# Performance work log

Measured on AMD Instinct MI355X. Metric: run time of the kernel, lower is better.

## Reference

```python
import jax, jax.numpy as jnp
import numpy as np

GD, D, S, L = 14, 128, 16, 2  # gaussian_dim, hidden_dim, d_state, num_layers


def _layernorm(x, g, b):
    m = x.mean(-1, keepdims=True)
    v = ((x - m) ** 2).mean(-1, keepdims=True)
    return (x - m) / jnp.sqrt(v + 1e-5) * g + b


def _scan_dir(x, dtW, dtb, BW, CW, Alog, Dskip):
    # x: [M, N, D]. Diagonal selective SSM, one direction.
    dt = jax.nn.softplus(x @ dtW + dtb)          # [M, N, D]
    Bm = x @ BW                                   # [M, N, S]
    Cm = x @ CW                                   # [M, N, S]
    A = -jnp.exp(Alog)                            # [D, S]

    def step(s, inp):
        x_t, dt_t, B_t, C_t = inp                 # [M,D],[M,D],[M,S],[M,S]
        s = jnp.exp(A * dt_t[:, :, None]) * s + (dt_t * x_t)[:, :, None] * B_t[:, None, :]
        y = jnp.einsum('mds,ms->md', s, C_t) + Dskip * x_t
        return s, y

    s0 = jnp.zeros((x.shape[0], D, S), x.dtype)
    _, ys = jax.lax.scan(step, s0, (x.transpose(1, 0, 2), dt.transpose(1, 0, 2),
                                    Bm.transpose(1, 0, 2), Cm.transpose(1, 0, 2)))
    return ys.transpose(1, 0, 2)                  # [M, N, D]


def setup_inputs() -> dict:
    key = jax.random.key(0)
    ks = jax.random.split(key, 20)
    N, B, P = 8, 1, 20000
    inp = {}
    inp['xyz'] = jax.random.normal(ks[0], (N, B, P, 3), jnp.float32)
    inp['scale'] = jax.random.normal(ks[1], (N, B, P, 3), jnp.float32)
    inp['rotation'] = jax.random.normal(ks[2], (N, B, P, 4), jnp.float32)
    inp['opacity'] = jax.random.normal(ks[3], (N, B, P, 1), jnp.float32)
    inp['color'] = jax.random.normal(ks[4], (N, B, P, 3), jnp.float32)
    inp['t'] = jnp.array([0.37], jnp.float32)
    inp['timestamps'] = jnp.linspace(0.0, 1.0, N, dtype=jnp.float32)

    def lin(k, i, o):
        return (jax.random.normal(k, (i, o), jnp.float32) / np.sqrt(i)).astype(jnp.float32)

    inp['in_W'] = lin(ks[5], GD, D); inp['in_b'] = jnp.zeros((D,), jnp.float32)
    inp['ln_g'] = jnp.ones((L, D), jnp.float32); inp['ln_b'] = jnp.zeros((L, D), jnp.float32)
    inp['dt_W'] = jax.random.normal(ks[6], (L, 2, D, D), jnp.float32) / np.sqrt(D)
    inp['dt_b'] = jnp.zeros((L, 2, D), jnp.float32)
    inp['B_W'] = jax.random.normal(ks[7], (L, 2, D, S), jnp.float32) / np.sqrt(D)
    inp['C_W'] = jax.random.normal(ks[8], (L, 2, D, S), jnp.float32) / np.sqrt(D)
    inp['A_log'] = jnp.log(jax.random.uniform(ks[9], (L, 2, D, S), jnp.float32, 0.5, 2.0))
    inp['D_skip'] = jnp.ones((L, 2, D), jnp.float32)
    inp['out_W'] = jax.random.normal(ks[10], (L, 2 * D, D), jnp.float32) / np.sqrt(2 * D)
    inp['out_b'] = jnp.zeros((L, D), jnp.float32)
    inp['te_W1'] = jax.random.normal(ks[11], (1, D), jnp.float32)
    inp['te_b1'] = jnp.zeros((D,), jnp.float32)
    inp['te_W2'] = jax.random.normal(ks[12], (D, D), jnp.float32) / np.sqrt(D)
    inp['te_b2'] = jnp.zeros((D,), jnp.float32)
    inp['op_W'] = jax.random.normal(ks[13], (D, GD), jnp.float32) / np.sqrt(D)
    inp['op_b'] = jnp.zeros((GD,), jnp.float32)
    return inp


def reference(xyz, scale, rotation, opacity, color, t, timestamps,
              in_W, in_b, ln_g, ln_b, dt_W, dt_b, B_W, C_W, A_log, D_skip,
              out_W, out_b, te_W1, te_b1, te_W2, te_b2, op_W, op_b):
    N, B, P = xyz.shape[0], xyz.shape[1], xyz.shape[2]
    M = B * P
    # stack frames: [N,B,P,14] -> [B*P, N, 14]
    params = jnp.concatenate([xyz, scale, rotation, opacity, color], -1)
    params = params.transpose(1, 2, 0, 3).reshape(M, N, GD)
    h = params @ in_W + in_b                      # [M, N, D]
    # sinusoidal temporal position encoding from continuous timestamps
    ts = jnp.broadcast_to(timestamps[None, :], (M, N))
    half = D // 2
    freqs = jnp.exp(-jnp.log(10000.0) * jnp.arange(half, dtype=h.dtype) / half)
    ang = ts[..., None] * freqs                   # [M, N, D/2]
    h = h + jnp.concatenate([jnp.sin(ang), jnp.cos(ang)], -1)
    # bidirectional SSM layers (pre-LN, residual)
    for l in range(L):
        xn = _layernorm(h, ln_g[l], ln_b[l])
        yf = _scan_dir(xn, dt_W[l, 0], dt_b[l, 0], B_W[l, 0], C_W[l, 0], A_log[l, 0], D_skip[l, 0])
        yb = jnp.flip(_scan_dir(jnp.flip(xn, 1), dt_W[l, 1], dt_b[l, 1], B_W[l, 1], C_W[l, 1],
                                A_log[l, 1], D_skip[l, 1]), 1)
        h = h + jnp.concatenate([yf, yb], -1) @ out_W[l] + out_b[l]
    # temporal query: linear interpolation between neighboring hidden states
    t_full = jnp.broadcast_to(t.reshape(B, 1), (B, P)).reshape(M)
    tn = t_full * (N - 1)
    idx_low = jnp.clip(jnp.floor(tn).astype(jnp.int32), 0, N - 2)
    idx_high = jnp.minimum(idx_low + 1, N - 1)
    alpha = (tn - idx_low.astype(h.dtype))[:, None]
    rows = jnp.arange(M)
    h_low = h[rows, idx_low]                      # [M, D]
    h_high = h[rows, idx_high]
    h_i = (1.0 - alpha) * h_low + alpha * h_high
    te = jax.nn.silu(t_full[:, None] @ te_W1 + te_b1) @ te_W2 + te_b2
    h_i = h_i + te
    out = (h_i @ op_W + op_b).reshape(B, P, GD)
    xyz_o = out[..., :3]
    scale_o = jax.nn.softplus(out[..., 3:6])
    rot = out[..., 6:10]
    rot_o = rot / jnp.clip(jnp.linalg.norm(rot, axis=-1, keepdims=True), 1e-12)
    opac_o = jax.nn.sigmoid(out[..., 10:11])
    col_o = jax.nn.sigmoid(out[..., 11:14])
    # dict fields concatenated in canonical order -> [B, P, 14]
    return jnp.concatenate([xyz_o, scale_o, rot_o, opac_o, col_o], -1)
```

## Files before the change

### kernel.cpp

```cpp
#include <hip/hip_runtime.h>
#include <math.h>

#define DD   128
#define SS   16
#define NL   2
#define GDIM 14
#define NN   8

typedef short  s16x8 __attribute__((ext_vector_type(8)));
typedef float  f32x4 __attribute__((ext_vector_type(4)));
typedef unsigned short ushort_t;

#define WS_INW   0
#define WS_DTW   4096
#define WS_BCW   69632
#define WS_OUTW  86016
#define WS_USH   151552
#define WS_AFLT  8192
#define WS_PEB   8192
#define WS_TE    9216

#if __has_builtin(__builtin_amdgcn_exp2f)
#define EXP2(x) __builtin_amdgcn_exp2f(x)
#else
#define EXP2(x) exp2f(x)
#endif

__device__ __forceinline__ unsigned short f2bf(float f) {
    unsigned u = __float_as_uint(f);
    u += 0x7fffu + ((u >> 16) & 1u);
    return (unsigned short)(u >> 16);
}

__device__ __forceinline__ float softplus_fast(float x) {
    return fmaxf(x, 0.f) + __logf(1.f + __expf(-fabsf(x)));
}
__device__ __forceinline__ float softplus_precise(float x) {
    return fmaxf(x, 0.f) + log1pf(expf(-fabsf(x)));
}

extern "C" __global__ void __launch_bounds__(256)
prep_weights(const float* __restrict__ inW, const float* __restrict__ dtW,
             const float* __restrict__ BW,  const float* __restrict__ CW,
             const float* __restrict__ outW, const float* __restrict__ Alog,
             const float* __restrict__ tstamp, const float* __restrict__ inB,
             const float* __restrict__ t_arr,
             const float* __restrict__ teW1, const float* __restrict__ teB1,
             const float* __restrict__ teW2, const float* __restrict__ teB2,
             int Bcnt, ushort_t* __restrict__ ws)
{
    float* wsf = (float*)(ws + WS_USH);
    int i = blockIdx.x * 256 + threadIdx.x;
    if (i < 4096) {
        int d = i >> 5, k = i & 31;
        ws[WS_INW + i] = (k < GDIM) ? f2bf(inW[k * DD + d]) : (ushort_t)0;
        return;
    }
    i -= 4096;
    if (i < 65536) {
        int l = i >> 15, r = i & 32767;
        int col = r >> 7, k = r & 127;
        int dir = col >> 7, d = col & 127;
        ws[WS_DTW + i] = f2bf(dtW[((size_t)(l * 2 + dir) * DD + k) * DD + d]);
        return;
    }
    i -= 65536;
    if (i < 16384) {
        int l = i >> 13, r = i & 8191;
        int col = r >> 7, k = r & 127;
        int dir = col >> 5, which = (col >> 4) & 1, s = col & 15;
        const float* Wsrc = which ? CW : BW;
        ws[WS_BCW + i] = f2bf(Wsrc[((size_t)(l * 2 + dir) * DD + k) * SS + s]);
        return;
    }
    i -= 16384;
    if (i < 65536) {
        int l = i >> 15, r = i & 32767;
        int col = r >> 8, k = r & 255;
        ws[WS_OUTW + i] = f2bf(outW[((size_t)l * 2 * DD + k) * DD + col]);
        return;
    }
    i -= 65536;
    if (i < WS_AFLT) {
        int ld = i >> 11, r = i & 2047;
        int s = r >> 7, d = r & 127;
        wsf[i] = -expf(Alog[((size_t)ld * DD + d) * SS + s]) * 1.44269504088896f;
        return;
    }
    i -= WS_AFLT;
    if (i < 1024) {
        int n = i >> 7, d = i & 127;
        int j = d & 63;
        float freq = expf(-logf(10000.f) * (float)j * (1.f / 64.f));
        float ang = tstamp[n] * freq;
        wsf[WS_PEB + i] = inB[d] + ((d < 64) ? sinf(ang) : cosf(ang));
        return;
    }
    i -= 1024;
    if (i < Bcnt * 128) {
        int b = i >> 7, d = i & 127;
        float tv = t_arr[b];
        float acc = teB2[d];
        for (int k = 0; k < DD; ++k) {
            float u = fmaf(tv, teW1[k], teB1[k]);
            float s = u / (1.f + expf(-u));
            acc = fmaf(s, teW2[k * DD + d], acc);
        }
        wsf[WS_TE + i] = acc;
    }
}

extern "C" __global__ void __launch_bounds__(256, 5)
ssm_mfma(const float* __restrict__ xyz, const float* __restrict__ scl,
         const float* __restrict__ rotp, const float* __restrict__ opa,
         const float* __restrict__ colp,
         const float* __restrict__ t_arr,
         const float* __restrict__ lnG, const float* __restrict__ lnB,
         const float* __restrict__ dtB,
         const float* __restrict__ Dskp,
         const float* __restrict__ outB,
         const float* __restrict__ opW, const float* __restrict__ opB,
         const ushort_t* __restrict__ wsu,
         float* __restrict__ out, int M, int Pb)
{
    const int t    = threadIdx.x;
    const int lane = t & 63;
    const int wv   = t >> 6;
    const int d    = t & 127;
    const int p    = t >> 7;
    const int m0   = blockIdx.x * 2;
    const int m    = m0 + p;
    const int r16  = lane & 15;
    const int kg   = lane >> 4;

    __shared__ float arenaA[16][132];
    __shared__ float arenaB[16][260];
    __shared__ float red  [4][2][NN];

    float (*pres)[132] = arenaA;
    ushort_t* XsU = (ushort_t*)&arenaA[0][0];
    float (*bcres)[68] = (float(*)[68])&arenaA[0][0];
    float (*dtres)[260] = arenaB;
    ushort_t* YsU = (ushort_t*)&arenaB[0][0];

    const ushort_t* inWt  = wsu + WS_INW;
    const ushort_t* dtWt  = wsu + WS_DTW;
    const ushort_t* bcWt  = wsu + WS_BCW;
    const ushort_t* outWt = wsu + WS_OUTW;
    const float*    wsf   = (const float*)(wsu + WS_USH);
    const float*    Apre  = wsf;
    const float*    peb   = wsf + WS_PEB;
    const float*    te    = wsf + WS_TE;

    for (int idx = t; idx < 16 * 32; idx += 256) {
        const int row = idx >> 5, k = idx & 31;
        const int pp = row >> 3, n = row & 7;
        const int mm = m0 + pp;
        float v = 0.f;
        if (k < GDIM && mm < M) {
            if (k < 3)       v = xyz [((size_t)n * M + mm) * 3 + k];
            else if (k < 6)  v = scl [((size_t)n * M + mm) * 3 + (k - 3)];
            else if (k < 10) v = rotp[((size_t)n * M + mm) * 4 + (k - 6)];
            else if (k < 11) v = opa [ (size_t)n * M + mm];
            else             v = colp[((size_t)n * M + mm) * 3 + (k - 11)];
        }
        XsU[row * 264 + k] = f2bf(v);
    }
    __syncthreads();

    {
        const s16x8 a = *(const s16x8*)&XsU[r16 * 264 + kg * 8];
        __syncthreads();
        #pragma unroll
        for (int ti = 0; ti < 2; ++ti) {
            const int col = (wv * 2 + ti) * 16 + r16;
            const s16x8 b = *(const s16x8*)&inWt[col * 32 + kg * 8];
            f32x4 acc = {0.f, 0.f, 0.f, 0.f};
            acc = __builtin_amdgcn_mfma_f32_16x16x32_bf16(a, b, acc, 0, 0, 0);
            #pragma unroll
            for (int j = 0; j < 4; ++j) pres[kg * 4 + j][col] = acc[j];
        }
    }
    __syncthreads();

    float h[NN];
    #pragma unroll
    for (int n = 0; n < NN; ++n)
        h[n] = pres[p * 8 + n][d] + peb[n * DD + d];

    for (int l = 0; l < NL; ++l) {
        float sum[NN], sq[NN];
        #pragma unroll
        for (int n = 0; n < NN; ++n) { sum[n] = h[n]; sq[n] = h[n] * h[n]; }
        #pragma unroll
        for (int off = 32; off > 0; off >>= 1) {
            #pragma unroll
            for (int n = 0; n < NN; ++n) {
                sum[n] += __shfl_xor(sum[n], off);
                sq[n]  += __shfl_xor(sq[n],  off);
            }
        }
        if (lane == 0) {
            #pragma unroll
            for (int n = 0; n < NN; ++n) { red[wv][0][n] = sum[n]; red[wv][1][n] = sq[n]; }
        }
        __syncthreads();

        float xn[NN];
        {
            const float gg = lnG[l * DD + d], bb = lnB[l * DD + d];
            #pragma unroll
            for (int n = 0; n < NN; ++n) {
                const float s0 = red[2 * p][0][n] + red[2 * p + 1][0][n];
                const float s1 = red[2 * p][1][n] + red[2 * p + 1][1][n];
                const float mean = s0 * (1.f / 128.f);
                float var = s1 * (1.f / 128.f) - mean * mean;
                const float inv = rsqrtf(fmaxf(var, 0.f) + 1e-5f);
                xn[n] = fmaf((h[n] - mean) * inv, gg, bb);
                XsU[(p * 8 + n) * 264 + d] = f2bf(xn[n]);
            }
        }
        __syncthreads();

        {
            s16x8 a[4];
            #pragma unroll
            for (int kc = 0; kc < 4; ++kc)
                a[kc] = *(const s16x8*)&XsU[r16 * 264 + kc * 32 + kg * 8];
            __syncthreads();

            const ushort_t* dtl = dtWt + l * 32768;
            #pragma unroll
            for (int ti = 0; ti < 4; ++ti) {
                const int col = (wv * 4 + ti) * 16 + r16;
                f32x4 acc = {0.f, 0.f, 0.f, 0.f};
                #pragma unroll
                for (int kc = 0; kc < 4; ++kc) {
                    const s16x8 b = *(const s16x8*)&dtl[col * 128 + kc * 32 + kg * 8];
                    acc = __builtin_amdgcn_mfma_f32_16x16x32_bf16(a[kc], b, acc, 0, 0, 0);
                }
                #pragma unroll
                for (int j = 0; j < 4; ++j) dtres[kg * 4 + j][col] = acc[j];
            }
            const ushort_t* bcl = bcWt + l * 8192;
            {
                const int col = wv * 16 + r16;
                f32x4 acc = {0.f, 0.f, 0.f, 0.f};
                #pragma unroll
                for (int kc = 0; kc < 4; ++kc) {
                    const s16x8 b = *(const s16x8*)&bcl[col * 128 + kc * 32 + kg * 8];
                    acc = __builtin_amdgcn_mfma_f32_16x16x32_bf16(a[kc], b, acc, 0, 0, 0);
                }
                #pragma unroll
                for (int j = 0; j < 4; ++j) bcres[kg * 4 + j][col] = acc[j];
            }
        }
        __syncthreads();

        float dtv[2][NN];
        #pragma unroll
        for (int dir = 0; dir < 2; ++dir) {
            const float db = dtB[(l * 2 + dir) * DD + d];
            #pragma unroll
            for (int n = 0; n < NN; ++n)
                dtv[dir][n] = softplus_fast(dtres[p * 8 + n][dir * 128 + d] + db);
        }
        __syncthreads();

        #pragma unroll
        for (int dir = 0; dir < 2; ++dir) {
            const float* Ap = Apre + (size_t)(l * 2 + dir) * SS * DD + d;
            float Ar[SS];
            #pragma unroll
            for (int s = 0; s < SS; ++s) Ar[s] = Ap[s * DD];
            const float dsk = Dskp[(l * 2 + dir) * DD + d];
            float st[SS];
            #pragma unroll
            for (int s = 0; s < SS; ++s) st[s] = 0.f;
            #pragma unroll
            for (int t8 = 0; t8 < NN; ++t8) {
                const int n = dir ? (NN - 1 - t8) : t8;
                const float dtc = dtv[dir][n];
                const float xv  = xn[n];
                const float dx  = dtc * xv;
                float y = dsk * xv;
                const float* base = &bcres[p * 8 + n][dir * 32];
                #pragma unroll
                for (int s4 = 0; s4 < SS; s4 += 4) {
                    const float4 Bv = *(const float4*)&base[s4];
                    const float4 Cv = *(const float4*)&base[16 + s4];
                    st[s4+0] = fmaf(EXP2(Ar[s4+0] * dtc), st[s4+0], dx * Bv.x);
                    y = fmaf(st[s4+0], Cv.x, y);
                    st[s4+1] = fmaf(EXP2(Ar[s4+1] * dtc), st[s4+1], dx * Bv.y);
                    y = fmaf(st[s4+1], Cv.y, y);
                    st[s4+2] = fmaf(EXP2(Ar[s4+2] * dtc), st[s4+2], dx * Bv.z);
                    y = fmaf(st[s4+2], Cv.z, y);
                    st[s4+3] = fmaf(EXP2(Ar[s4+3] * dtc), st[s4+3], dx * Bv.w);
                    y = fmaf(st[s4+3], Cv.w, y);
                }
                YsU[(p * 8 + n) * 520 + dir * 128 + d] = f2bf(y);
            }
        }
        __syncthreads();

        {
            s16x8 a[8];
            #pragma unroll
            for (int kc = 0; kc < 8; ++kc)
                a[kc] = *(const s16x8*)&YsU[r16 * 520 + kc * 32 + kg * 8];
            const ushort_t* ol = outWt + l * 32768;
            #pragma unroll
            for (int ti = 0; ti < 2; ++ti) {
                const int col = (wv * 2 + ti) * 16 + r16;
                f32x4 acc = {0.f, 0.f, 0.f, 0.f};
                #pragma unroll
                for (int kc = 0; kc < 8; ++kc) {
                    const s16x8 b = *(const s16x8*)&ol[col * 256 + kc * 32 + kg * 8];
                    acc = __builtin_amdgcn_mfma_f32_16x16x32_bf16(a[kc], b, acc, 0, 0, 0);
                }
                #pragma unroll
                for (int j = 0; j < 4; ++j) pres[kg * 4 + j][col] = acc[j];
            }
        }
        __syncthreads();

        {
            const float ob = outB[l * DD + d];
            #pragma unroll
            for (int n = 0; n < NN; ++n) h[n] += pres[p * 8 + n][d] + ob;
        }
    }

    const int mc = (m < M) ? m : (M - 1);
    const int bidx = mc / Pb;
    const float tv = t_arr[bidx];
    const float tn = tv * (float)(NN - 1);
    int il = (int)floorf(tn);
    il = il < 0 ? 0 : (il > NN - 2 ? NN - 2 : il);
    const float alpha = tn - (float)il;
    float hlow = 0.f, hhigh = 0.f;
    #pragma unroll
    for (int n = 0; n < NN; ++n) {
        if (n == il)     hlow  = h[n];
        if (n == il + 1) hhigh = h[n];
    }
    float hi = (1.f - alpha) * hlow + alpha * hhigh + te[bidx * DD + d];

    float* epi = &arenaB[0][0];
    epi[p * 132 + d] = hi;
    __syncthreads();

    if (d < GDIM * 8) {
        const int g = d >> 3, j = d & 7;
        float part = 0.f;
        #pragma unroll
        for (int q = 0; q < 16; ++q)
            part = fmaf(epi[p * 132 + j + 8 * q], opW[(j + 8 * q) * GDIM + g], part);
        part += __shfl_xor(part, 4);
        part += __shfl_xor(part, 2);
        part += __shfl_xor(part, 1);
        if (j == 0) epi[264 + p * 16 + g] = part + opB[g];
    }
    __syncthreads();

    if (d < GDIM && m < M) {
        const int g = d;
        const float v = epi[264 + p * 16 + g];
        float r;
        if (g < 3)        r = v;
        else if (g < 6)   r = softplus_precise(v);
        else if (g < 10) {
            const float q0 = epi[264 + p * 16 + 6], q1 = epi[264 + p * 16 + 7];
            const float q2 = epi[264 + p * 16 + 8], q3 = epi[264 + p * 16 + 9];
            const float nrm = sqrtf(fmaf(q0,q0, fmaf(q1,q1, fmaf(q2,q2, q3*q3))));
            r = v / fmaxf(nrm, 1e-12f);
        } else {
            r = 1.f / (1.f + expf(-v));
        }
        out[(size_t)m * GDIM + g] = r;
    }
}

extern "C" void kernel_launch(void* const* d_in, const int* in_sizes, int n_in,
                              void* d_out, int out_size, void* d_ws, size_t ws_size,
                              hipStream_t stream) {
    const float* xyz   = (const float*)d_in[0];
    const float* scl   = (const float*)d_in[1];
    const float* rotp  = (const float*)d_in[2];
    const float* opa   = (const float*)d_in[3];
    const float* colp  = (const float*)d_in[4];
    const float* t_arr = (const float*)d_in[5];
    const float* tstmp = (const float*)d_in[6];
    const float* inW   = (const float*)d_in[7];
    const float* inB   = (const float*)d_in[8];
    const float* lnG   = (const float*)d_in[9];
    const float* lnB   = (const float*)d_in[10];
    const float* dtW   = (const float*)d_in[11];
    const float* dtB   = (const float*)d_in[12];
    const float* BW    = (const float*)d_in[13];
    const float* CW    = (const float*)d_in[14];
    const float* Alog  = (const float*)d_in[15];
    const float* Dskp  = (const float*)d_in[16];
    const float* outW  = (const float*)d_in[17];
    const float* outB  = (const float*)d_in[18];
    const float* teW1  = (const float*)d_in[19];
    const float* teB1  = (const float*)d_in[20];
    const float* teW2  = (const float*)d_in[21];
    const float* teB2  = (const float*)d_in[22];
    const float* opW   = (const float*)d_in[23];
    const float* opB   = (const float*)d_in[24];

    const int N  = in_sizes[6];
    const int M  = in_sizes[3] / N;
    const int B  = in_sizes[5];
    const int Pb = M / B;
    (void)N; (void)out_size; (void)n_in;

    ushort_t* wsu = (ushort_t*)d_ws;
    const int prep_elems = WS_USH + WS_AFLT + 1024 + B * 128;
    hipLaunchKernelGGL(prep_weights, dim3((prep_elems + 255) / 256), dim3(256), 0, stream,
                       inW, dtW, BW, CW, outW, Alog, tstmp, inB, t_arr,
                       teW1, teB1, teW2, teB2, B, wsu);
    hipLaunchKernelGGL(ssm_mfma, dim3((M + 1) / 2), dim3(256), 0, stream,
                       xyz, scl, rotp, opa, colp, t_arr,
                       lnG, lnB, dtB, Dskp, outB, opW, opB,
                       wsu, (float*)d_out, M, Pb);
}
```

Baseline: 591.0 us.

## Split fused SSM kernel into staged front, scan, mid, and tail kernels

Replaces the single fused per-point kernel with a pipeline of five launches (front projection and layernorm, per-layer scan, mid out-projection and layernorm, tail interpolation and head). Intermediates such as hidden state, normalized input, dt, B/C and scan outputs go through global scratch in the workspace, processed in chunks that fit the available space. The aim is to let each stage run at its own occupancy and register budget instead of one heavy kernel. The cost is extra global memory traffic and more kernel launches. The original fused kernel is kept as a fallback when the workspace is too small.

New measurement: 801.2 us. +35.6%, slower.

```diff
diff --git a/kernel.cpp b/kernel.cpp
--- a/kernel.cpp
+++ b/kernel.cpp
@@ -31,7 +31,9 @@
     u += 0x7fffu + ((u >> 16) & 1u);
     return (unsigned short)(u >> 16);
 }
-
+__device__ __forceinline__ float bf2f(ushort_t u) {
+    return __uint_as_float(((unsigned)u) << 16);
+}
 __device__ __forceinline__ float softplus_fast(float x) {
     return fmaxf(x, 0.f) + __logf(1.f + __expf(-fabsf(x)));
 }
@@ -110,18 +112,481 @@
     }
 }
 
-extern "C" __global__ void __launch_bounds__(256, 5)
-ssm_mfma(const float* __restrict__ xyz, const float* __restrict__ scl,
+
+extern "C" __global__ void __launch_bounds__(256, 4)
+k1_front(const float* __restrict__ xyz, const float* __restrict__ scl,
          const float* __restrict__ rotp, const float* __restrict__ opa,
          const float* __restrict__ colp,
-         const float* __restrict__ t_arr,
          const float* __restrict__ lnG, const float* __restrict__ lnB,
-         const float* __restrict__ dtB,
-         const float* __restrict__ Dskp,
-         const float* __restrict__ outB,
-         const float* __restrict__ opW, const float* __restrict__ opB,
          const ushort_t* __restrict__ wsu,
-         float* __restrict__ out, int M, int Pb)
+         float* __restrict__ Hb, ushort_t* __restrict__ XNb,
+         float* __restrict__ DTb, float* __restrict__ BCb,
+         int M, int Mc, int m_off)
+{
+    const int t    = threadIdx.x;
+    const int lane = t & 63;
+    const int wv   = t >> 6;
+    const int d    = t & 127;
+    const int p    = t >> 7;
+    const int lm0  = blockIdx.x * 2;
+    const int lm   = lm0 + p;
+    const int m0   = m_off + lm0;
+    const int r16  = lane & 15;
+    const int kg   = lane >> 4;
+
+    __shared__ float arenaA[16][132];
+    __shared__ float red[4][2][NN];
+    float (*pres)[132] = arenaA;
+    ushort_t* XsU = (ushort_t*)&arenaA[0][0];
+
+    const ushort_t* inWt = wsu + WS_INW;
+    const ushort_t* dtWt = wsu + WS_DTW;
+    const ushort_t* bcWt = wsu + WS_BCW;
+    const float*    wsf  = (const float*)(wsu + WS_USH);
+    const float*    peb  = wsf + WS_PEB;
+
+    for (int idx = t; idx < 16 * 32; idx += 256) {
+        const int row = idx >> 5, k = idx & 31;
+        const int pp = row >> 3, n = row & 7;
+        const int mm = m0 + pp;
+        float v = 0.f;
+        if (k < GDIM && mm < M) {
+            if (k < 3)       v = xyz [((size_t)n * M + mm) * 3 + k];
+            else if (k < 6)  v = scl [((size_t)n * M + mm) * 3 + (k - 3)];
+            else if (k < 10) v = rotp[((size_t)n * M + mm) * 4 + (k - 6)];
+            else if (k < 11) v = opa [ (size_t)n * M + mm];
+            else             v = colp[((size_t)n * M + mm) * 3 + (k - 11)];
+        }
+        XsU[row * 264 + k] = f2bf(v);
+    }
+    __syncthreads();
+
+    {
+        const s16x8 a = *(const s16x8*)&XsU[r16 * 264 + kg * 8];
+        __syncthreads();
+        #pragma unroll
+        for (int ti = 0; ti < 2; ++ti) {
+            const int col = (wv * 2 + ti) * 16 + r16;
+            const s16x8 b = *(const s16x8*)&inWt[col * 32 + kg * 8];
+            f32x4 acc = {0.f, 0.f, 0.f, 0.f};
+            acc = __builtin_amdgcn_mfma_f32_16x16x32_bf16(a, b, acc, 0, 0, 0);
+            #pragma unroll
+            for (int j = 0; j < 4; ++j) pres[kg * 4 + j][col] = acc[j];
+        }
+    }
+    __syncthreads();
+
+    float h[NN];
+    #pragma unroll
+    for (int n = 0; n < NN; ++n) {
+        h[n] = pres[p * 8 + n][d] + peb[n * DD + d];
+        Hb[((size_t)n * Mc + lm) * DD + d] = h[n];
+    }
+
+    float sum[NN], sq[NN];
+    #pragma unroll
+    for (int n = 0; n < NN; ++n) { sum[n] = h[n]; sq[n] = h[n] * h[n]; }
+    #pragma unroll
+    for (int off = 32; off > 0; off >>= 1) {
+        #pragma unroll
+        for (int n = 0; n < NN; ++n) {
+            sum[n] += __shfl_xor(sum[n], off);
+            sq[n]  += __shfl_xor(sq[n],  off);
+        }
+    }
+    if (lane == 0) {
+        #pragma unroll
+        for (int n = 0; n < NN; ++n) { red[wv][0][n] = sum[n]; red[wv][1][n] = sq[n]; }
+    }
+    __syncthreads();
+
+    {
+        const float gg = lnG[d], bb = lnB[d];
+        #pragma unroll
+        for (int n = 0; n < NN; ++n) {
+            const float s0 = red[2 * p][0][n] + red[2 * p + 1][0][n];
+            const float s1 = red[2 * p][1][n] + red[2 * p + 1][1][n];
+            const float mean = s0 * (1.f / 128.f);
+            float var = s1 * (1.f / 128.f) - mean * mean;
+            const float inv = rsqrtf(fmaxf(var, 0.f) + 1e-5f);
+            const float xnv = fmaf((h[n] - mean) * inv, gg, bb);
+            const ushort_t xb = f2bf(xnv);
+            XsU[(p * 8 + n) * 264 + d] = xb;
+            XNb[((size_t)n * Mc + lm) * DD + d] = xb;
+        }
+    }
+    __syncthreads();
+
+    {
+        s16x8 a[4];
+        #pragma unroll
+        for (int kc = 0; kc < 4; ++kc)
+            a[kc] = *(const s16x8*)&XsU[r16 * 264 + kc * 32 + kg * 8];
+
+        const ushort_t* dtl = dtWt;
+        #pragma unroll
+        for (int ti = 0; ti < 4; ++ti) {
+            const int col = (wv * 4 + ti) * 16 + r16;
+            f32x4 acc = {0.f, 0.f, 0.f, 0.f};
+            #pragma unroll
+            for (int kc = 0; kc < 4; ++kc) {
+                const s16x8 b = *(const s16x8*)&dtl[col * 128 + kc * 32 + kg * 8];
+                acc = __builtin_amdgcn_mfma_f32_16x16x32_bf16(a[kc], b, acc, 0, 0, 0);
+            }
+            #pragma unroll
+            for (int j = 0; j < 4; ++j) {
+                const int row = kg * 4 + j;
+                const int lmr = lm0 + (row >> 3), nr = row & 7;
+                DTb[((size_t)nr * Mc + lmr) * 256 + col] = acc[j];
+            }
+        }
+        const ushort_t* bcl = bcWt;
+        {
+            const int col = wv * 16 + r16;
+            f32x4 acc = {0.f, 0.f, 0.f, 0.f};
+            #pragma unroll
+            for (int kc = 0; kc < 4; ++kc) {
+                const s16x8 b = *(const s16x8*)&bcl[col * 128 + kc * 32 + kg * 8];
+                acc = __builtin_amdgcn_mfma_f32_16x16x32_bf16(a[kc], b, acc, 0, 0, 0);
+            }
+            #pragma unroll
+            for (int j = 0; j < 4; ++j) {
+                const int row = kg * 4 + j;
+                const int lmr = lm0 + (row >> 3), nr = row & 7;
+                BCb[((size_t)lmr * 8 + nr) * 64 + col] = acc[j];
+            }
+        }
+    }
+}
+
+extern "C" __global__ void __launch_bounds__(256, 5)
+k2_scan(const ushort_t* __restrict__ wsu,
+        const ushort_t* __restrict__ XNb, const float* __restrict__ DTb,
+        const float* __restrict__ BCb, ushort_t* __restrict__ YB,
+        const float* __restrict__ dtB, const float* __restrict__ Dskp,
+        int Mc, int l)
+{
+    const int t  = threadIdx.x;
+    const int d  = t & 127;
+    const int p  = t >> 7;
+    const int lm = blockIdx.x * 2 + p;
+
+    __shared__ float bcs[1024];
+    {
+        float4* dst = (float4*)bcs;
+        const float4* src = (const float4*)(BCb + (size_t)blockIdx.x * 1024);
+        dst[t] = src[t];
+    }
+    __syncthreads();
+
+    const float* wsf  = (const float*)(wsu + WS_USH);
+    const float* Apre = wsf;
+
+    float dtv[2][NN];
+    #pragma unroll
+    for (int dir = 0; dir < 2; ++dir) {
+        const float db = dtB[(l * 2 + dir) * DD + d];
+        #pragma unroll
+        for (int n = 0; n < NN; ++n)
+            dtv[dir][n] = softplus_fast(DTb[((size_t)n * Mc + lm) * 256 + dir * 128 + d] + db);
+    }
+    float xn[NN];
+    #pragma unroll
+    for (int n = 0; n < NN; ++n)
+        xn[n] = bf2f(XNb[((size_t)n * Mc + lm) * DD + d]);
+
+    #pragma unroll
+    for (int dir = 0; dir < 2; ++dir) {
+        const float* Ap = Apre + (size_t)(l * 2 + dir) * SS * DD + d;
+        float Ar[SS];
+        #pragma unroll
+        for (int s = 0; s < SS; ++s) Ar[s] = Ap[s * DD];
+        const float dsk = Dskp[(l * 2 + dir) * DD + d];
+        float st[SS];
+        #pragma unroll
+        for (int s = 0; s < SS; ++s) st[s] = 0.f;
+        #pragma unroll
+        for (int t8 = 0; t8 < NN; ++t8) {
+            const int n = dir ? (NN - 1 - t8) : t8;
+            const float dtc = dtv[dir][n];
+            const float xv  = xn[n];
+            const float dx  = dtc * xv;
+            float y = dsk * xv;
+            const float* base = &bcs[p * 512 + n * 64 + dir * 32];
+            #pragma unroll
+            for (int s4 = 0; s4 < SS; s4 += 4) {
+                const float4 Bv = *(const float4*)&base[s4];
+                const float4 Cv = *(const float4*)&base[16 + s4];
+                st[s4+0] = fmaf(EXP2(Ar[s4+0] * dtc), st[s4+0], dx * Bv.x);
+                y = fmaf(st[s4+0], Cv.x, y);
+                st[s4+1] = fmaf(EXP2(Ar[s4+1] * dtc), st[s4+1], dx * Bv.y);
+                y = fmaf(st[s4+1], Cv.y, y);
+                st[s4+2] = fmaf(EXP2(Ar[s4+2] * dtc), st[s4+2], dx * Bv.z);
+                y = fmaf(st[s4+2], Cv.z, y);
+                st[s4+3] = fmaf(EXP2(Ar[s4+3] * dtc), st[s4+3], dx * Bv.w);
+                y = fmaf(st[s4+3], Cv.w, y);
+            }
+            YB[((size_t)n * Mc + lm) * 256 + dir * 128 + d] = f2bf(y);
+        }
+    }
+}
+
+extern "C" __global__ void __launch_bounds__(256, 4)
+k3_mid(const ushort_t* __restrict__ wsu,
+       float* __restrict__ Hb, ushort_t* __restrict__ XNb,
+       float* __restrict__ DTb, float* __restrict__ BCb,
+       const ushort_t* __restrict__ YB,
+       const float* __restrict__ outB,
+       const float* __restrict__ lnG, const float* __restrict__ lnB,
+       int Mc, int lout, int lin)
+{
+    const int t    = threadIdx.x;
+    const int lane = t & 63;
+    const int wv   = t >> 6;
+    const int d    = t & 127;
+    const int p    = t >> 7;
+    const int lm0  = blockIdx.x * 2;
+    const int lm   = lm0 + p;
+    const int r16  = lane & 15;
+    const int kg   = lane >> 4;
+
+    __shared__ float arenaA[16][132];
+    __shared__ float red[4][2][NN];
+    float (*pres)[132] = arenaA;
+    ushort_t* XsU = (ushort_t*)&arenaA[0][0];
+
+    const ushort_t* dtWt  = wsu + WS_DTW;
+    const ushort_t* bcWt  = wsu + WS_BCW;
+    const ushort_t* outWt = wsu + WS_OUTW;
+
+    {
+        const int prow = r16 >> 3, nrow = r16 & 7;
+        const size_t grow = (size_t)nrow * Mc + (lm0 + prow);
+        s16x8 a[8];
+        #pragma unroll
+        for (int kc = 0; kc < 8; ++kc)
+            a[kc] = *(const s16x8*)&YB[grow * 256 + kc * 32 + kg * 8];
+        const ushort_t* ol = outWt + lout * 32768;
+        #pragma unroll
+        for (int ti = 0; ti < 2; ++ti) {
+            const int col = (wv * 2 + ti) * 16 + r16;
+            f32x4 acc = {0.f, 0.f, 0.f, 0.f};
+            #pragma unroll
+            for (int kc = 0; kc < 8; ++kc) {
+                const s16x8 b = *(const s16x8*)&ol[col * 256 + kc * 32 + kg * 8];
+                acc = __builtin_amdgcn_mfma_f32_16x16x32_bf16(a[kc], b, acc, 0, 0, 0);
+            }
+            #pragma unroll
+            for (int j = 0; j < 4; ++j) pres[kg * 4 + j][col] = acc[j];
+        }
+    }
+    __syncthreads();
+
+    float h[NN];
+    {
+        const float ob = outB[lout * DD + d];
+        #pragma unroll
+        for (int n = 0; n < NN; ++n) {
+            h[n] = Hb[((size_t)n * Mc + lm) * DD + d] + pres[p * 8 + n][d] + ob;
+            Hb[((size_t)n * Mc + lm) * DD + d] = h[n];
+        }
+    }
+
+    float sum[NN], sq[NN];
+    #pragma unroll
+    for (int n = 0; n < NN; ++n) { sum[n] = h[n]; sq[n] = h[n] * h[n]; }
+    #pragma unroll
+    for (int off = 32; off > 0; off >>= 1) {
+        #pragma unroll
+        for (int n = 0; n < NN; ++n) {
+            sum[n] += __shfl_xor(sum[n], off);
+            sq[n]  += __shfl_xor(sq[n],  off);
+        }
+    }
+    if (lane == 0) {
+        #pragma unroll
+        for (int n = 0; n < NN; ++n) { red[wv][0][n] = sum[n]; red[wv][1][n] = sq[n]; }
+    }
+    __syncthreads();
+
+    {
+        const float gg = lnG[lin * DD + d], bb = lnB[lin * DD + d];
+        #pragma unroll
+        for (int n = 0; n < NN; ++n) {
+            const float s0 = red[2 * p][0][n] + red[2 * p + 1][0][n];
+            const float s1 = red[2 * p][1][n] + red[2 * p + 1][1][n];
+            const float mean = s0 * (1.f / 128.f);
+            float var = s1 * (1.f / 128.f) - mean * mean;
+            const float inv = rsqrtf(fmaxf(var, 0.f) + 1e-5f);
+            const float xnv = fmaf((h[n] - mean) * inv, gg, bb);
+            const ushort_t xb = f2bf(xnv);
+            XsU[(p * 8 + n) * 264 + d] = xb;
+            XNb[((size_t)n * Mc + lm) * DD + d] = xb;
+        }
+    }
+    __syncthreads();
+
+    {
+        s16x8 a[4];
+        #pragma unroll
+        for (int kc = 0; kc < 4; ++kc)
+            a[kc] = *(const s16x8*)&XsU[r16 * 264 + kc * 32 + kg * 8];
+
+        const ushort_t* dtl = dtWt + lin * 32768;
+        #pragma unroll
+        for (int ti = 0; ti < 4; ++ti) {
+            const int col = (wv * 4 + ti) * 16 + r16;
+            f32x4 acc = {0.f, 0.f, 0.f, 0.f};
+            #pragma unroll
+            for (int kc = 0; kc < 4; ++kc) {
+                const s16x8 b = *(const s16x8*)&dtl[col * 128 + kc * 32 + kg * 8];
+                acc = __builtin_amdgcn_mfma_f32_16x16x32_bf16(a[kc], b, acc, 0, 0, 0);
+            }
+            #pragma unroll
+            for (int j = 0; j < 4; ++j) {
+                const int row = kg * 4 + j;
+                const int lmr = lm0 + (row >> 3), nr = row & 7;
+                DTb[((size_t)nr * Mc + lmr) * 256 + col] = acc[j];
+            }
+        }
+        const ushort_t* bcl = bcWt + lin * 8192;
+        {
+            const int col = wv * 16 + r16;
+            f32x4 acc = {0.f, 0.f, 0.f, 0.f};
+            #pragma unroll
+            for (int kc = 0; kc < 4; ++kc) {
+                const s16x8 b = *(const s16x8*)&bcl[col * 128 + kc * 32 + kg * 8];
+                acc = __builtin_amdgcn_mfma_f32_16x16x32_bf16(a[kc], b, acc, 0, 0, 0);
+            }
+            #pragma unroll
+            for (int j = 0; j < 4; ++j) {
+                const int row = kg * 4 + j;
+                const int lmr = lm0 + (row >> 3), nr = row & 7;
+                BCb[((size_t)lmr * 8 + nr) * 64 + col] = acc[j];
+            }
+        }
+    }
+}
+
+extern "C" __global__ void __launch_bounds__(256, 4)
+k5_tail(const ushort_t* __restrict__ wsu,
+        const float* __restrict__ Hb, const ushort_t* __restrict__ YB,
+        const float* __restrict__ outB, const float* __restrict__ t_arr,
+        const float* __restrict__ opW, const float* __restrict__ opB,
+        float* __restrict__ out, int M, int Mc, int m_off, int Pb, int lout)
+{
+    const int t    = threadIdx.x;
+    const int lane = t & 63;
+    const int wv   = t >> 6;
+    const int d    = t & 127;
+    const int p    = t >> 7;
+    const int lm0  = blockIdx.x * 2;
+    const int lm   = lm0 + p;
+    const int m    = m_off + lm;
+    const int r16  = lane & 15;
+    const int kg   = lane >> 4;
+
+    __shared__ float arenaA[16][132];
+    float (*pres)[132] = arenaA;
+    float* epi = &arenaA[0][0];
+
+    const ushort_t* outWt = wsu + WS_OUTW;
+    const float*    wsf   = (const float*)(wsu + WS_USH);
+    const float*    te    = wsf + WS_TE;
+
+    {
+        const int prow = r16 >> 3, nrow = r16 & 7;
+        const size_t grow = (size_t)nrow * Mc + (lm0 + prow);
+        s16x8 a[8];
+        #pragma unroll
+        for (int kc = 0; kc < 8; ++kc)
+            a[kc] = *(const s16x8*)&YB[grow * 256 + kc * 32 + kg * 8];
+        const ushort_t* ol = outWt + lout * 32768;
+        #pragma unroll
+        for (int ti = 0; ti < 2; ++ti) {
+            const int col = (wv * 2 + ti) * 16 + r16;
+            f32x4 acc = {0.f, 0.f, 0.f, 0.f};
+            #pragma unroll
+            for (int kc = 0; kc < 8; ++kc) {
+                const s16x8 b = *(const s16x8*)&ol[col * 256 + kc * 32 + kg * 8];
+                acc = __builtin_amdgcn_mfma_f32_16x16x32_bf16(a[kc], b, acc, 0, 0, 0);
+            }
+            #pragma unroll
+            for (int j = 0; j < 4; ++j) pres[kg * 4 + j][col] = acc[j];
+        }
+    }
+    __syncthreads();
+
+    float h[NN];
+    {
+        const float ob = outB[lout * DD + d];
+        #pragma unroll
+        for (int n = 0; n < NN; ++n)
+            h[n] = Hb[((size_t)n * Mc + lm) * DD + d] + pres[p * 8 + n][d] + ob;
+    }
+
+    const int mc_   = (m < M) ? m : (M - 1);
+    const int bidx  = mc_ / Pb;
+    const float tv  = t_arr[bidx];
+    const float tn  = tv * (float)(NN - 1);
+    int il = (int)floorf(tn);
+    il = il < 0 ? 0 : (il > NN - 2 ? NN - 2 : il);
+    const float alpha = tn - (float)il;
+    float hlow = 0.f, hhigh = 0.f;
+    #pragma unroll
+    for (int n = 0; n < NN; ++n) {
+        if (n == il)     hlow  = h[n];
+        if (n == il + 1) hhigh = h[n];
+    }
+    float hi = (1.f - alpha) * hlow + alpha * hhigh + te[bidx * DD + d];
+
+    __syncthreads();
+    epi[p * 132 + d] = hi;
+    __syncthreads();
+
+    if (d < GDIM * 8) {
+        const int g = d >> 3, j = d & 7;
+        float part = 0.f;
+        #pragma unroll
+        for (int q = 0; q < 16; ++q)
+            part = fmaf(epi[p * 132 + j + 8 * q], opW[(j + 8 * q) * GDIM + g], part);
+        part += __shfl_xor(part, 4);
+        part += __shfl_xor(part, 2);
+        part += __shfl_xor(part, 1);
+        if (j == 0) epi[264 + p * 16 + g] = part + opB[g];
+    }
+    __syncthreads();
+
+    if (d < GDIM && m < M) {
+        const int g = d;
+        const float v = epi[264 + p * 16 + g];
+        float r;
+        if (g < 3)        r = v;
+        else if (g < 6)   r = softplus_precise(v);
+        else if (g < 10) {
+            const float q0 = epi[264 + p * 16 + 6], q1 = epi[264 + p * 16 + 7];
+            const float q2 = epi[264 + p * 16 + 8], q3 = epi[264 + p * 16 + 9];
+            const float nrm = sqrtf(fmaf(q0,q0, fmaf(q1,q1, fmaf(q2,q2, q3*q3))));
+            r = v / fmaxf(nrm, 1e-12f);
+        } else {
+            r = 1.f / (1.f + expf(-v));
+        }
+        out[(size_t)m * GDIM + g] = r;
+    }
+}
+
+extern "C" __global__ void __launch_bounds__(256, 4)
+ssm_fused_fb(const float* __restrict__ xyz, const float* __restrict__ scl,
+             const float* __restrict__ rotp, const float* __restrict__ opa,
+             const float* __restrict__ colp,
+             const float* __restrict__ t_arr,
+             const float* __restrict__ lnG, const float* __restrict__ lnB,
+             const float* __restrict__ dtB,
+             const float* __restrict__ Dskp,
+             const float* __restrict__ outB,
+             const float* __restrict__ opW, const float* __restrict__ opB,
+             const ushort_t* __restrict__ wsu,
+             float* __restrict__ out, int M, int Pb)
 {
     const int t    = threadIdx.x;
     const int lane = t & 63;
@@ -417,12 +882,50 @@
     (void)N; (void)out_size; (void)n_in;
 
     ushort_t* wsu = (ushort_t*)d_ws;
+
     const int prep_elems = WS_USH + WS_AFLT + 1024 + B * 128;
     hipLaunchKernelGGL(prep_weights, dim3((prep_elems + 255) / 256), dim3(256), 0, stream,
                        inW, dtW, BW, CW, outW, Alog, tstmp, inB, t_arr,
                        teW1, teB1, teW2, teB2, B, wsu);
-    hipLaunchKernelGGL(ssm_mfma, dim3((M + 1) / 2), dim3(256), 0, stream,
-                       xyz, scl, rotp, opa, colp, t_arr,
-                       lnG, lnB, dtB, Dskp, outB, opW, opB,
-                       wsu, (float*)d_out, M, Pb);
-}
+
+    const size_t fixed_bytes  = 303104 + (size_t)(WS_AFLT + 1024 + (size_t)B * 128) * 4;
+    const size_t scratch_off  = (fixed_bytes + 4095) & ~(size_t)4095;
+    const size_t per_pt       = 4096 + 2048 + 8192 + 2048 + 4096;
+    const size_t avail        = ws_size > scratch_off ? ws_size - scratch_off : 0;
+    const int    M_even       = (M + 1) & ~1;
+    size_t mc_cap = avail / per_pt;
+    if (mc_cap > (size_t)M_even) mc_cap = (size_t)M_even;
+    int Mc = (int)(mc_cap & ~(size_t)1);
+
+    if (Mc >= 2048 || Mc >= M_even) {
+        char* s = (char*)d_ws + scratch_off;
+        float*    Hb  = (float*)s;
+        ushort_t* XNb = (ushort_t*)(s + (size_t)Mc * 4096);
+        float*    DTb = (float*)(s + (size_t)Mc * 6144);
+        float*    BCb = (float*)(s + (size_t)Mc * 14336);
+        ushort_t* YB  = (ushort_t*)(s + (size_t)Mc * 16384);
+
+        for (int off = 0; off < M; off += Mc) {
+            const int Mcur = (M - off < Mc) ? (M - off) : Mc;
+            const int Me   = (Mcur + 1) & ~1;
+            const int nb   = Me / 2;
+            hipLaunchKernelGGL(k1_front, dim3(nb), dim3(256), 0, stream,
+                               xyz, scl, rotp, opa, colp, lnG, lnB, wsu,
+                               Hb, XNb, DTb, BCb, M, Mc, off);
+            hipLaunchKernelGGL(k2_scan, dim3(nb), dim3(256), 0, stream,
+                               wsu, XNb, DTb, BCb, YB, dtB, Dskp, Mc, 0);
+            hipLaunchKernelGGL(k3_mid, dim3(nb), dim3(256), 0, stream,
+                               wsu, Hb, XNb, DTb, BCb, YB, outB, lnG, lnB, Mc, 0, 1);
+            hipLaunchKernelGGL(k2_scan, dim3(nb), dim3(256), 0, stream,
+                               wsu, XNb, DTb, BCb, YB, dtB, Dskp, Mc, 1);
+            hipLaunchKernelGGL(k5_tail, dim3(nb), dim3(256), 0, stream,
+                               wsu, Hb, YB, outB, t_arr, opW, opB,
+                               (float*)d_out, M, Mc, off, Pb, 1);
+        }
+    } else {
+        hipLaunchKernelGGL(ssm_fused_fb, dim3((M + 1) / 2), dim3(256), 0, stream,
+                           xyz, scl, rotp, opa, colp, t_arr,
+                           lnG, lnB, dtB, Dskp, outB, opW, opB,
+                           wsu, (float*)d_out, M, Pb);
+    }
+}
```

## Process one particle per 128-thread block instead of two per 256-thread block

Applied to the files above, without the earlier changes.

Each block now handles a single particle sequence, launching M blocks of 128 threads with halved shared-memory arenas. The MFMA A operand duplicates the 8 valid rows into the 16-row tile, and only half the result rows are stored. The aim is smaller blocks and lower shared-memory use, for more resident blocks and finer scheduling. The cost is that half of every matrix-core tile is wasted, and weight loads per particle double.

After: 737.5 us. 24.8% more time.

```diff
diff --git a/kernel.cpp b/kernel.cpp
--- a/kernel.cpp
+++ b/kernel.cpp
@@ -110,7 +110,7 @@
     }
 }
 
-extern "C" __global__ void __launch_bounds__(256, 5)
+extern "C" __global__ void __launch_bounds__(128, 4)
 ssm_mfma(const float* __restrict__ xyz, const float* __restrict__ scl,
          const float* __restrict__ rotp, const float* __restrict__ opa,
          const float* __restrict__ colp,
@@ -126,16 +126,15 @@
     const int t    = threadIdx.x;
     const int lane = t & 63;
     const int wv   = t >> 6;
-    const int d    = t & 127;
-    const int p    = t >> 7;
-    const int m0   = blockIdx.x * 2;
-    const int m    = m0 + p;
+    const int d    = t;
+    const int m    = blockIdx.x;
     const int r16  = lane & 15;
+    const int r8   = lane & 7;
     const int kg   = lane >> 4;
 
-    __shared__ float arenaA[16][132];
-    __shared__ float arenaB[16][260];
-    __shared__ float red  [4][2][NN];
+    __shared__ float arenaA[8][132];
+    __shared__ float arenaB[8][260];
+    __shared__ float red  [2][2][NN];
 
     float (*pres)[132] = arenaA;
     ushort_t* XsU = (ushort_t*)&arenaA[0][0];
@@ -152,33 +151,33 @@
     const float*    peb   = wsf + WS_PEB;
     const float*    te    = wsf + WS_TE;
 
-    for (int idx = t; idx < 16 * 32; idx += 256) {
-        const int row = idx >> 5, k = idx & 31;
-        const int pp = row >> 3, n = row & 7;
-        const int mm = m0 + pp;
+    for (int idx = t; idx < 8 * 32; idx += 128) {
+        const int n = idx >> 5, k = idx & 31;
         float v = 0.f;
-        if (k < GDIM && mm < M) {
-            if (k < 3)       v = xyz [((size_t)n * M + mm) * 3 + k];
-            else if (k < 6)  v = scl [((size_t)n * M + mm) * 3 + (k - 3)];
-            else if (k < 10) v = rotp[((size_t)n * M + mm) * 4 + (k - 6)];
-            else if (k < 11) v = opa [ (size_t)n * M + mm];
-            else             v = colp[((size_t)n * M + mm) * 3 + (k - 11)];
-        }
-        XsU[row * 264 + k] = f2bf(v);
+        if (k < GDIM && m < M) {
+            if (k < 3)       v = xyz [((size_t)n * M + m) * 3 + k];
+            else if (k < 6)  v = scl [((size_t)n * M + m) * 3 + (k - 3)];
+            else if (k < 10) v = rotp[((size_t)n * M + m) * 4 + (k - 6)];
+            else if (k < 11) v = opa [ (size_t)n * M + m];
+            else             v = colp[((size_t)n * M + m) * 3 + (k - 11)];
+        }
+        XsU[n * 264 + k] = f2bf(v);
     }
     __syncthreads();
 
     {
-        const s16x8 a = *(const s16x8*)&XsU[r16 * 264 + kg * 8];
-        __syncthreads();
-        #pragma unroll
-        for (int ti = 0; ti < 2; ++ti) {
-            const int col = (wv * 2 + ti) * 16 + r16;
+        const s16x8 a = *(const s16x8*)&XsU[r8 * 264 + kg * 8];
+        __syncthreads();
+        #pragma unroll
+        for (int ti = 0; ti < 4; ++ti) {
+            const int col = (wv * 4 + ti) * 16 + r16;
             const s16x8 b = *(const s16x8*)&inWt[col * 32 + kg * 8];
             f32x4 acc = {0.f, 0.f, 0.f, 0.f};
             acc = __builtin_amdgcn_mfma_f32_16x16x32_bf16(a, b, acc, 0, 0, 0);
-            #pragma unroll
-            for (int j = 0; j < 4; ++j) pres[kg * 4 + j][col] = acc[j];
+            if (kg < 2) {
+                #pragma unroll
+                for (int j = 0; j < 4; ++j) pres[kg * 4 + j][col] = acc[j];
+            }
         }
     }
     __syncthreads();
@@ -186,7 +185,7 @@
     float h[NN];
     #pragma unroll
     for (int n = 0; n < NN; ++n)
-        h[n] = pres[p * 8 + n][d] + peb[n * DD + d];
+        h[n] = pres[n][d] + peb[n * DD + d];
 
     for (int l = 0; l < NL; ++l) {
         float sum[NN], sq[NN];
@@ -211,13 +210,13 @@
             const float gg = lnG[l * DD + d], bb = lnB[l * DD + d];
             #pragma unroll
             for (int n = 0; n < NN; ++n) {
-                const float s0 = red[2 * p][0][n] + red[2 * p + 1][0][n];
-                const float s1 = red[2 * p][1][n] + red[2 * p + 1][1][n];
+                const float s0 = red[0][0][n] + red[1][0][n];
+                const float s1 = red[0][1][n] + red[1][1][n];
                 const float mean = s0 * (1.f / 128.f);
                 float var = s1 * (1.f / 128.f) - mean * mean;
                 const float inv = rsqrtf(fmaxf(var, 0.f) + 1e-5f);
                 xn[n] = fmaf((h[n] - mean) * inv, gg, bb);
-                XsU[(p * 8 + n) * 264 + d] = f2bf(xn[n]);
+                XsU[n * 264 + d] = f2bf(xn[n]);
             }
         }
         __syncthreads();
@@ -226,33 +225,38 @@
             s16x8 a[4];
             #pragma unroll
             for (int kc = 0; kc < 4; ++kc)
-                a[kc] = *(const s16x8*)&XsU[r16 * 264 + kc * 32 + kg * 8];
+                a[kc] = *(const s16x8*)&XsU[r8 * 264 + kc * 32 + kg * 8];
             __syncthreads();
 
             const ushort_t* dtl = dtWt + l * 32768;
             #pragma unroll
-            for (int ti = 0; ti < 4; ++ti) {
-                const int col = (wv * 4 + ti) * 16 + r16;
+            for (int ti = 0; ti < 8; ++ti) {
+                const int col = (wv * 8 + ti) * 16 + r16;
                 f32x4 acc = {0.f, 0.f, 0.f, 0.f};
                 #pragma unroll
                 for (int kc = 0; kc < 4; ++kc) {
                     const s16x8 b = *(const s16x8*)&dtl[col * 128 + kc * 32 + kg * 8];
                     acc = __builtin_amdgcn_mfma_f32_16x16x32_bf16(a[kc], b, acc, 0, 0, 0);
                 }
-                #pragma unroll
-                for (int j = 0; j < 4; ++j) dtres[kg * 4 + j][col] = acc[j];
+                if (kg < 2) {
+                    #pragma unroll
+                    for (int j = 0; j < 4; ++j) dtres[kg * 4 + j][col] = acc[j];
+                }
             }
             const ushort_t* bcl = bcWt + l * 8192;
-            {
-                const int col = wv * 16 + r16;
+            #pragma unroll
+            for (int ti = 0; ti < 2; ++ti) {
+                const int col = (wv * 2 + ti) * 16 + r16;
                 f32x4 acc = {0.f, 0.f, 0.f, 0.f};
                 #pragma unroll
                 for (int kc = 0; kc < 4; ++kc) {
                     const s16x8 b = *(const s16x8*)&bcl[col * 128 + kc * 32 + kg * 8];
                     acc = __builtin_amdgcn_mfma_f32_16x16x32_bf16(a[kc], b, acc, 0, 0, 0);
                 }
-                #pragma unroll
-                for (int j = 0; j < 4; ++j) bcres[kg * 4 + j][col] = acc[j];
+                if (kg < 2) {
+                    #pragma unroll
+                    for (int j = 0; j < 4; ++j) bcres[kg * 4 + j][col] = acc[j];
+                }
             }
         }
         __syncthreads();
@@ -263,7 +267,7 @@
             const float db = dtB[(l * 2 + dir) * DD + d];
             #pragma unroll
             for (int n = 0; n < NN; ++n)
-                dtv[dir][n] = softplus_fast(dtres[p * 8 + n][dir * 128 + d] + db);
+                dtv[dir][n] = softplus_fast(dtres[n][dir * 128 + d] + db);
         }
         __syncthreads();
 
@@ -284,7 +288,7 @@
                 const float xv  = xn[n];
                 const float dx  = dtc * xv;
                 float y = dsk * xv;
-                const float* base = &bcres[p * 8 + n][dir * 32];
+                const float* base = &bcres[n][dir * 32];
                 #pragma unroll
                 for (int s4 = 0; s4 < SS; s4 += 4) {
                     const float4 Bv = *(const float4*)&base[s4];
@@ -298,7 +302,7 @@
                     st[s4+3] = fmaf(EXP2(Ar[s4+3] * dtc), st[s4+3], dx * Bv.w);
                     y = fmaf(st[s4+3], Cv.w, y);
                 }
-                YsU[(p * 8 + n) * 520 + dir * 128 + d] = f2bf(y);
+                YsU[n * 520 + dir * 128 + d] = f2bf(y);
             }
         }
         __syncthreads();
@@ -307,19 +311,21 @@
             s16x8 a[8];
             #pragma unroll
             for (int kc = 0; kc < 8; ++kc)
-                a[kc] = *(const s16x8*)&YsU[r16 * 520 + kc * 32 + kg * 8];
+                a[kc] = *(const s16x8*)&YsU[r8 * 520 + kc * 32 + kg * 8];
             const ushort_t* ol = outWt + l * 32768;
             #pragma unroll
-            for (int ti = 0; ti < 2; ++ti) {
-                const int col = (wv * 2 + ti) * 16 + r16;
+            for (int ti = 0; ti < 4; ++ti) {
+                const int col = (wv * 4 + ti) * 16 + r16;
                 f32x4 acc = {0.f, 0.f, 0.f, 0.f};
                 #pragma unroll
                 for (int kc = 0; kc < 8; ++kc) {
                     const s16x8 b = *(const s16x8*)&ol[col * 256 + kc * 32 + kg * 8];
                     acc = __builtin_amdgcn_mfma_f32_16x16x32_bf16(a[kc], b, acc, 0, 0, 0);
                 }
-                #pragma unroll
-                for (int j = 0; j < 4; ++j) pres[kg * 4 + j][col] = acc[j];
+                if (kg < 2) {
+                    #pragma unroll
+                    for (int j = 0; j < 4; ++j) pres[kg * 4 + j][col] = acc[j];
+                }
             }
         }
         __syncthreads();
@@ -327,7 +333,7 @@
         {
             const float ob = outB[l * DD + d];
             #pragma unroll
-            for (int n = 0; n < NN; ++n) h[n] += pres[p * 8 + n][d] + ob;
+            for (int n = 0; n < NN; ++n) h[n] += pres[n][d] + ob;
         }
     }
 
@@ -347,7 +353,7 @@
     float hi = (1.f - alpha) * hlow + alpha * hhigh + te[bidx * DD + d];
 
     float* epi = &arenaB[0][0];
-    epi[p * 132 + d] = hi;
+    epi[d] = hi;
     __syncthreads();
 
     if (d < GDIM * 8) {
@@ -355,23 +361,23 @@
         float part = 0.f;
         #pragma unroll
         for (int q = 0; q < 16; ++q)
-            part = fmaf(epi[p * 132 + j + 8 * q], opW[(j + 8 * q) * GDIM + g], part);
+            part = fmaf(epi[j + 8 * q], opW[(j + 8 * q) * GDIM + g], part);
         part += __shfl_xor(part, 4);
         part += __shfl_xor(part, 2);
         part += __shfl_xor(part, 1);
-        if (j == 0) epi[264 + p * 16 + g] = part + opB[g];
+        if (j == 0) epi[132 + g] = part + opB[g];
     }
     __syncthreads();
 
     if (d < GDIM && m < M) {
         const int g = d;
-        const float v = epi[264 + p * 16 + g];
+        const float v = epi[132 + g];
         float r;
         if (g < 3)        r = v;
         else if (g < 6)   r = softplus_precise(v);
         else if (g < 10) {
-            const float q0 = epi[264 + p * 16 + 6], q1 = epi[264 + p * 16 + 7];
-            const float q2 = epi[264 + p * 16 + 8], q3 = epi[264 + p * 16 + 9];
+            const float q0 = epi[132 + 6], q1 = epi[132 + 7];
+            const float q2 = epi[132 + 8], q3 = epi[132 + 9];
             const float nrm = sqrtf(fmaf(q0,q0, fmaf(q1,q1, fmaf(q2,q2, q3*q3))));
             r = v / fmaxf(nrm, 1e-12f);
         } else {
@@ -421,7 +427,7 @@
     hipLaunchKernelGGL(prep_weights, dim3((prep_elems + 255) / 256), dim3(256), 0, stream,
                        inW, dtW, BW, CW, outW, Alog, tstmp, inB, t_arr,
                        teW1, teB1, teW2, teB2, B, wsu);
-    hipLaunchKernelGGL(ssm_mfma, dim3((M + 1) / 2), dim3(256), 0, stream,
+    hipLaunchKernelGGL(ssm_mfma, dim3(M), dim3(128), 0, stream,
                        xyz, scl, rotp, opa, colp, t_arr,
                        lnG, lnB, dtB, Dskp, outB, opW, opB,
                        wsu, (float*)d_out, M, Pb);
```
